# Kernel optimization log

Hardware: AMD Instinct MI355X
Metric: run time of the kernel (lower is better)

## Reference

```python
import jax, jax.numpy as jnp
import numpy as np


def _gather_neighbors(v, idx):
    # v: [B, N, D], idx: [B, N, K] -> [B, N, K, D]
    return jax.vmap(lambda vb, ib: vb[ib])(v, idx)


def setup_inputs() -> dict:
    key = jax.random.key(0)
    B, N, P, D, K = 8, 2048, 64, 128, 16
    ks = jax.random.split(key, 24)
    s = lambda fan_in: 1.0 / np.sqrt(fan_in)
    inp = {
        "x": jax.random.normal(ks[0], (B, N, 3), jnp.float32),
        "in_f": jax.random.normal(ks[1], (B, N, P), jnp.float32),
        "W_fc1": jax.random.normal(ks[2], (P, D), jnp.float32) * s(P),
        "b_fc1": jnp.zeros((D,), jnp.float32),
        "W_phi": jax.random.normal(ks[3], (D, D), jnp.float32) * s(D),
        "W_psi": jax.random.normal(ks[4], (D, D), jnp.float32) * s(D),
        "W_alpha": jax.random.normal(ks[5], (D, D), jnp.float32) * s(D),
        "W_dpt1": jax.random.normal(ks[6], (D, D), jnp.float32) * s(D),
        "b_dpt1": jnp.zeros((D,), jnp.float32),
        "W_dpt2": jax.random.normal(ks[7], (D, D), jnp.float32) * s(D),
        "b_dpt2": jnp.zeros((D,), jnp.float32),
        "W_gam1": jax.random.normal(ks[8], (D, D), jnp.float32) * s(D),
        "b_gam1": jnp.zeros((D,), jnp.float32),
        "W_gam2": jax.random.normal(ks[9], (D, D), jnp.float32) * s(D),
        "b_gam2": jnp.zeros((D,), jnp.float32),
        "W_del1": jax.random.normal(ks[10], (3, D), jnp.float32) * s(3),
        "b_del1": jnp.zeros((D,), jnp.float32),
        "W_del2": jax.random.normal(ks[11], (D, D), jnp.float32) * s(D),
        "b_del2": jnp.zeros((D,), jnp.float32),
        "W_fc2": jax.random.normal(ks[12], (D, P), jnp.float32) * s(D),
        "b_fc2": jnp.zeros((P,), jnp.float32),
        "k": K,
    }
    return inp


def reference(x, in_f, W_fc1, b_fc1, W_phi, W_psi, W_alpha,
              W_dpt1, b_dpt1, W_dpt2, b_dpt2,
              W_gam1, b_gam1, W_gam2, b_gam2,
              W_del1, b_del1, W_del2, b_del2,
              W_fc2, b_fc2, k):
    # squared pairwise distance [B, N, N] without [B,N,N,3] intermediate
    x2 = jnp.sum(x * x, axis=-1)                      # [B, N]
    d2 = x2[:, :, None] + x2[:, None, :] - 2.0 * jnp.einsum('bnc,bmc->bnm', x, x)
    knn_idx = jnp.argsort(d2, axis=-1)[:, :, :k]       # [B, N, K]

    points_knn = _gather_neighbors(x, knn_idx)         # [B, N, K, 3]
    f = in_f @ W_fc1 + b_fc1                           # [B, N, D]

    # positional encoding delta: MLP(x_i - x_j)
    diff = x[:, :, None, :] - points_knn               # [B, N, K, 3]
    delta = jax.nn.relu(diff @ W_del1 + b_del1) @ W_del2 + b_del2  # [B,N,K,D]

    psi = _gather_neighbors(f @ W_psi, knn_idx)        # [B, N, K, D]
    phi = (f @ W_phi)[:, :, None, :]                   # [B, N, 1, D]
    alpha = _gather_neighbors(f @ W_alpha, knn_idx)    # [B, N, K, D]
    dropped = (jax.nn.relu(f @ W_dpt1 + b_dpt1) @ W_dpt2 + b_dpt2)[:, :, None, :]

    pre = phi - psi + delta + dropped                  # [B, N, K, D]
    gamma = jax.nn.relu(pre @ W_gam1 + b_gam1) @ W_gam2 + b_gam2
    rho = jax.nn.softmax(gamma / jnp.sqrt(jnp.float32(k)), axis=2)

    y = jnp.sum(rho * (alpha + delta), axis=2)         # [B, N, D]
    return y @ W_fc2 + b_fc2 + in_f
```

## Files before the change

kernel.cpp:

```cpp
#include <hip/hip_runtime.h>
#include <hip/hip_bf16.h>
#include <math.h>

#define Bq 8
#define Nq 2048
#define Pq 64
#define Dq 128
#define Kq 16
#define BNq (Bq * Nq)

typedef unsigned short u16;
typedef __bf16 bf16x8v __attribute__((ext_vector_type(8)));
typedef float f32x4v __attribute__((ext_vector_type(4)));

__device__ __forceinline__ u16 f2b(float f) {
    return __builtin_bit_cast(u16, (__bf16)f);
}

#define OFF_DEL2 0
#define OFF_GAM1 16384
#define OFF_GAM2 32768
#define OFF_FC1  49152
#define OFF_PHI  57344
#define OFF_PSI  73728
#define OFF_ALF  90112
#define OFF_DPT1 106496
#define OFF_DPT2 122880
#define WT_TOTAL 139264

__global__ __launch_bounds__(256) void prep_kernel(
    const float* __restrict__ Wdel2, const float* __restrict__ Wgam1,
    const float* __restrict__ Wgam2, const float* __restrict__ Wfc1,
    const float* __restrict__ Wphi, const float* __restrict__ Wpsi,
    const float* __restrict__ Walpha, const float* __restrict__ Wdpt1,
    const float* __restrict__ Wdpt2, u16* __restrict__ Wt) {
    int idx = blockIdx.x * 256 + threadIdx.x;
    const float* W;
    int n, k;
    if (idx < OFF_FC1) {
        int m = idx >> 14, r = idx & 16383;
        W = (m == 0) ? Wdel2 : (m == 1) ? Wgam1 : Wgam2;
        n = r >> 7; k = r & 127;
    } else if (idx < OFF_PHI) {
        int r = idx - OFF_FC1;
        W = Wfc1; n = r >> 6; k = r & 63;
    } else {
        int r = idx - OFF_PHI;
        int m = r >> 14; r &= 16383;
        W = (m == 0) ? Wphi : (m == 1) ? Wpsi : (m == 2) ? Walpha : (m == 3) ? Wdpt1 : Wdpt2;
        n = r >> 7; k = r & 127;
    }
    Wt[idx] = f2b(W[k * 128 + n]);
}

__global__ __launch_bounds__(512) void knn_kernel(const float* __restrict__ x,
                                                  int* __restrict__ knn) {
    __shared__ float4 sx[Nq];
    __shared__ float sLd[32][16][17];
    __shared__ u16   sLi[32][16][17];
    const int b = blockIdx.x >> 6;
    const int q0 = (blockIdx.x & 63) * 32;
    const float* xb = x + b * Nq * 3;
    for (int j = threadIdx.x; j < Nq; j += 512) {
        float x0 = xb[j * 3 + 0], x1 = xb[j * 3 + 1], x2 = xb[j * 3 + 2];
        float n2 = __fadd_rn(__fadd_rn(__fmul_rn(x0, x0), __fmul_rn(x1, x1)),
                             __fmul_rn(x2, x2));
        sx[j] = make_float4(x0, x1, x2, n2);
    }
    __syncthreads();
    const int q = threadIdx.x & 31;
    const int sub = threadIdx.x >> 5;
    const float4 qv = sx[q0 + q];
    float bd[Kq];
    int bj[Kq];
#pragma unroll
    for (int s = 0; s < Kq; ++s) { bd[s] = INFINITY; bj[s] = 0x7fff; }
    const int j0 = sub * 128;
    for (int i = 0; i < 128; ++i) {
        const int j = j0 + i;
        float4 p = sx[j];
        float dot = __fadd_rn(__fadd_rn(__fmul_rn(qv.x, p.x), __fmul_rn(qv.y, p.y)),
                              __fmul_rn(qv.z, p.z));
        float d = __fsub_rn(__fadd_rn(qv.w, p.w), __fmul_rn(2.0f, dot));
        if (d < bd[Kq - 1]) {
            bd[Kq - 1] = d; bj[Kq - 1] = j;
#pragma unroll
            for (int s = Kq - 1; s >= 1; --s) {
                if (bd[s] < bd[s - 1]) {
                    float td = bd[s]; bd[s] = bd[s - 1]; bd[s - 1] = td;
                    int tj = bj[s]; bj[s] = bj[s - 1]; bj[s - 1] = tj;
                }
            }
        }
    }
#pragma unroll
    for (int s = 0; s < Kq; ++s) { sLd[q][sub][s] = bd[s]; sLi[q][sub][s] = (u16)bj[s]; }
    __syncthreads();
    if (threadIdx.x < 256) {
        const int mq = threadIdx.x & 31;
        const int s2 = threadIdx.x >> 5;
        float md[Kq]; int mi[Kq];
        int pa = 0, pb = 0;
#pragma unroll
        for (int i = 0; i < Kq; ++i) {
            float da = sLd[mq][2 * s2][pa], db = sLd[mq][2 * s2 + 1][pb];
            int ia = sLi[mq][2 * s2][pa], ib = sLi[mq][2 * s2 + 1][pb];
            bool ta = (da < db) || (da == db && ia < ib);
            md[i] = ta ? da : db; mi[i] = ta ? ia : ib;
            if (ta) ++pa; else ++pb;
        }
#pragma unroll
        for (int i = 0; i < Kq; ++i) { sLd[mq][2 * s2][i] = md[i]; sLi[mq][2 * s2][i] = (u16)mi[i]; }
    }
    __syncthreads();
    if (threadIdx.x < 32) {
        const int mq = threadIdx.x;
        int pos[8]; float hd[8]; int hi[8];
#pragma unroll
        for (int s = 0; s < 8; ++s) {
            pos[s] = 1; hd[s] = sLd[mq][2 * s][0]; hi[s] = sLi[mq][2 * s][0];
        }
        int* o = knn + (b * Nq + q0 + mq) * Kq;
#pragma unroll
        for (int oi = 0; oi < Kq; ++oi) {
            float bdv = hd[0]; int biv = hi[0]; int bs = 0;
#pragma unroll
            for (int s = 1; s < 8; ++s) {
                bool take = (hd[s] < bdv) || (hd[s] == bdv && hi[s] < biv);
                if (take) { bdv = hd[s]; biv = hi[s]; bs = s; }
            }
            o[oi] = biv;
#pragma unroll
            for (int s = 0; s < 8; ++s) {
                if (s == bs) {
                    int pp = pos[s] < Kq ? pos[s] : (Kq - 1);
                    bool ok = pos[s] < Kq;
                    hd[s] = ok ? sLd[mq][2 * s][pp] : INFINITY;
                    hi[s] = ok ? sLi[mq][2 * s][pp] : 0x7fffffff;
                    pos[s]++;
                }
            }
        }
    }
}

template <int BYTES, int ROWBYTES>
__device__ __forceinline__ void stageW(const u16* __restrict__ src,
                                       u16* __restrict__ sW, int t) {
#pragma unroll
    for (int c = 0; c < BYTES / 4096; ++c) {
        int lin = c * 4096 + t * 16;
        int n = lin / ROWBYTES;
        int o = lin % ROWBYTES;
        bf16x8v v = *(const bf16x8v*)((const char*)src + lin);
        *(bf16x8v*)((char*)sW + n * ROWBYTES + (o ^ ((n & 7) << 4))) = v;
    }
}

__device__ __forceinline__ void mfma_k128(const u16* __restrict__ sA,
                                          const u16* __restrict__ sW,
                                          int colbase, int lane,
                                          f32x4v (&acc)[4][2]) {
    const int kg = lane >> 4;
    const int l15 = lane & 15;
#pragma unroll
    for (int ks = 0; ks < 4; ++ks) {
        bf16x8v a[4], bfr[2];
#pragma unroll
        for (int m = 0; m < 4; ++m) {
            int row = m * 16 + l15;
            int o = (ks * 64 + kg * 16) ^ ((row & 7) << 4);
            a[m] = *(const bf16x8v*)((const char*)sA + row * 256 + o);
        }
#pragma unroll
        for (int nt = 0; nt < 2; ++nt) {
            int n = colbase + nt * 16 + l15;
            int o = (ks * 64 + kg * 16) ^ ((n & 7) << 4);
            bfr[nt] = *(const bf16x8v*)((const char*)sW + n * 256 + o);
        }
#pragma unroll
        for (int m = 0; m < 4; ++m)
#pragma unroll
            for (int nt = 0; nt < 2; ++nt)
                acc[m][nt] = __builtin_amdgcn_mfma_f32_16x16x32_bf16(a[m], bfr[nt], acc[m][nt], 0, 0, 0);
    }
}

__device__ __forceinline__ void mfma_k64(const u16* __restrict__ sA,
                                         const u16* __restrict__ sW,
                                         int colbase, int lane,
                                         f32x4v (&acc)[4][2]) {
    const int kg = lane >> 4;
    const int l15 = lane & 15;
#pragma unroll
    for (int ks = 0; ks < 2; ++ks) {
        bf16x8v a[4], bfr[2];
#pragma unroll
        for (int m = 0; m < 4; ++m) {
            int row = m * 16 + l15;
            int o = (ks * 64 + kg * 16) ^ ((row & 7) << 4);
            a[m] = *(const bf16x8v*)((const char*)sA + row * 128 + o);
        }
#pragma unroll
        for (int nt = 0; nt < 2; ++nt) {
            int n = colbase + nt * 16 + l15;
            int o = (ks * 64 + kg * 16) ^ ((n & 7) << 4);
            bfr[nt] = *(const bf16x8v*)((const char*)sW + n * 128 + o);
        }
#pragma unroll
        for (int m = 0; m < 4; ++m)
#pragma unroll
            for (int nt = 0; nt < 2; ++nt)
                acc[m][nt] = __builtin_amdgcn_mfma_f32_16x16x32_bf16(a[m], bfr[nt], acc[m][nt], 0, 0, 0);
    }
}

__global__ __launch_bounds__(256, 2) void feat_kernel(
    const float* __restrict__ in_f, const u16* __restrict__ Wt,
    const float* __restrict__ bfc1, const float* __restrict__ bdpt1,
    const float* __restrict__ bdpt2,
    float* __restrict__ base, u16* __restrict__ psiB, u16* __restrict__ alphaB) {
    __shared__ __align__(16) u16 sIn[64 * 64];
    __shared__ __align__(16) u16 sF[64 * 128];
    __shared__ __align__(16) u16 sW[128 * 128];
    const int t = threadIdx.x;
    const int lane = t & 63;
    const int w = t >> 6;
    const int kg = lane >> 4;
    const int l15 = lane & 15;
    const int p0 = blockIdx.x * 64;

    {
        const int r = t >> 2;
        const int c0 = (t & 3) * 16;
        const float* src = &in_f[(size_t)(p0 + r) * 64 + c0];
        float4 v0 = *(const float4*)(src + 0);
        float4 v1 = *(const float4*)(src + 4);
        float4 v2 = *(const float4*)(src + 8);
        float4 v3 = *(const float4*)(src + 12);
        bf16x8v lo, hi;
        lo[0] = (__bf16)v0.x; lo[1] = (__bf16)v0.y; lo[2] = (__bf16)v0.z; lo[3] = (__bf16)v0.w;
        lo[4] = (__bf16)v1.x; lo[5] = (__bf16)v1.y; lo[6] = (__bf16)v1.z; lo[7] = (__bf16)v1.w;
        hi[0] = (__bf16)v2.x; hi[1] = (__bf16)v2.y; hi[2] = (__bf16)v2.z; hi[3] = (__bf16)v2.w;
        hi[4] = (__bf16)v3.x; hi[5] = (__bf16)v3.y; hi[6] = (__bf16)v3.z; hi[7] = (__bf16)v3.w;
        const int swz = (r & 7) << 4;
        *(bf16x8v*)((char*)sIn + r * 128 + ((c0 * 2) ^ swz)) = lo;
        *(bf16x8v*)((char*)sIn + r * 128 + (((c0 + 8) * 2) ^ swz)) = hi;
    }

    f32x4v acc[4][2], accPhi[4][2];

    {
        float bv0 = bfc1[w * 32 + l15];
        float bv1 = bfc1[w * 32 + 16 + l15];
#pragma unroll
        for (int m = 0; m < 4; ++m) { acc[m][0] = f32x4v{bv0, bv0, bv0, bv0}; acc[m][1] = f32x4v{bv1, bv1, bv1, bv1}; }
    }
    stageW<16384, 128>(Wt + OFF_FC1, sW, t);
    __syncthreads();
    mfma_k64(sIn, sW, w * 32, lane, acc);

#pragma unroll
    for (int m = 0; m < 4; ++m)
#pragma unroll
        for (int nt = 0; nt < 2; ++nt)
#pragma unroll
            for (int rr = 0; rr < 4; ++rr) {
                int row = m * 16 + kg * 4 + rr;
                int col = w * 32 + nt * 16 + l15;
                *(__bf16*)((char*)sF + row * 256 + ((col * 2) ^ ((row & 7) << 4))) = (__bf16)acc[m][nt][rr];
            }

#pragma unroll
    for (int m = 0; m < 4; ++m) { accPhi[m][0] = f32x4v{0, 0, 0, 0}; accPhi[m][1] = f32x4v{0, 0, 0, 0}; }
    __syncthreads();
    stageW<32768, 256>(Wt + OFF_PHI, sW, t);
    __syncthreads();
    mfma_k128(sF, sW, w * 32, lane, accPhi);

#pragma unroll
    for (int m = 0; m < 4; ++m) { acc[m][0] = f32x4v{0, 0, 0, 0}; acc[m][1] = f32x4v{0, 0, 0, 0}; }
    __syncthreads();
    stageW<32768, 256>(Wt + OFF_PSI, sW, t);
    __syncthreads();
    mfma_k128(sF, sW, w * 32, lane, acc);
#pragma unroll
    for (int m = 0; m < 4; ++m)
#pragma unroll
        for (int nt = 0; nt < 2; ++nt)
#pragma unroll
            for (int rr = 0; rr < 4; ++rr) {
                int row = m * 16 + kg * 4 + rr;
                int col = w * 32 + nt * 16 + l15;
                psiB[(size_t)(p0 + row) * 128 + col] = f2b(acc[m][nt][rr]);
            }

#pragma unroll
    for (int m = 0; m < 4; ++m) { acc[m][0] = f32x4v{0, 0, 0, 0}; acc[m][1] = f32x4v{0, 0, 0, 0}; }
    __syncthreads();
    stageW<32768, 256>(Wt + OFF_ALF, sW, t);
    __syncthreads();
    mfma_k128(sF, sW, w * 32, lane, acc);
#pragma unroll
    for (int m = 0; m < 4; ++m)
#pragma unroll
        for (int nt = 0; nt < 2; ++nt)
#pragma unroll
            for (int rr = 0; rr < 4; ++rr) {
                int row = m * 16 + kg * 4 + rr;
                int col = w * 32 + nt * 16 + l15;
                alphaB[(size_t)(p0 + row) * 128 + col] = f2b(acc[m][nt][rr]);
            }

    {
        float bv0 = bdpt1[w * 32 + l15];
        float bv1 = bdpt1[w * 32 + 16 + l15];
#pragma unroll
        for (int m = 0; m < 4; ++m) { acc[m][0] = f32x4v{bv0, bv0, bv0, bv0}; acc[m][1] = f32x4v{bv1, bv1, bv1, bv1}; }
    }
    __syncthreads();
    stageW<32768, 256>(Wt + OFF_DPT1, sW, t);
    __syncthreads();
    mfma_k128(sF, sW, w * 32, lane, acc);
    __syncthreads();
#pragma unroll
    for (int m = 0; m < 4; ++m)
#pragma unroll
        for (int nt = 0; nt < 2; ++nt)
#pragma unroll
            for (int rr = 0; rr < 4; ++rr) {
                int row = m * 16 + kg * 4 + rr;
                int col = w * 32 + nt * 16 + l15;
                *(__bf16*)((char*)sF + row * 256 + ((col * 2) ^ ((row & 7) << 4))) =
                    (__bf16)fmaxf(acc[m][nt][rr], 0.f);
            }

    {
        float bv0 = bdpt2[w * 32 + l15];
        float bv1 = bdpt2[w * 32 + 16 + l15];
#pragma unroll
        for (int m = 0; m < 4; ++m) { acc[m][0] = f32x4v{bv0, bv0, bv0, bv0}; acc[m][1] = f32x4v{bv1, bv1, bv1, bv1}; }
    }
    __syncthreads();
    stageW<32768, 256>(Wt + OFF_DPT2, sW, t);
    __syncthreads();
    mfma_k128(sF, sW, w * 32, lane, acc);
#pragma unroll
    for (int m = 0; m < 4; ++m)
#pragma unroll
        for (int nt = 0; nt < 2; ++nt)
#pragma unroll
            for (int rr = 0; rr < 4; ++rr) {
                int row = m * 16 + kg * 4 + rr;
                int col = w * 32 + nt * 16 + l15;
                base[(size_t)(p0 + row) * 128 + col] = acc[m][nt][rr] + accPhi[m][nt][rr];
            }
}

__device__ __forceinline__ void mfma_n1(const u16* __restrict__ sA,
                                        const u16* __restrict__ sW,
                                        int colW, int kg, int l15,
                                        f32x4v (&acc)[4]) {
#pragma unroll
    for (int ks = 0; ks < 4; ++ks) {
        bf16x8v a[4], bb;
#pragma unroll
        for (int m = 0; m < 4; ++m) {
            int row = m * 16 + l15;
            int o = (ks * 64 + kg * 16) ^ ((row & 7) << 4);
            a[m] = *(const bf16x8v*)((const char*)sA + row * 256 + o);
        }
        {
            int o = (ks * 64 + kg * 16) ^ ((colW & 7) << 4);
            bb = *(const bf16x8v*)((const char*)sW + colW * 256 + o);
        }
#pragma unroll
        for (int m = 0; m < 4; ++m)
            acc[m] = __builtin_amdgcn_mfma_f32_16x16x32_bf16(a[m], bb, acc[m], 0, 0, 0);
    }
}

__global__ __launch_bounds__(512, 1) void main_kernel(
    const float* __restrict__ x, const float* __restrict__ in_f,
    const float* __restrict__ Wdel1, const float* __restrict__ bdel1,
    const float* __restrict__ bdel2,
    const float* __restrict__ bgam1, const float* __restrict__ bgam2,
    const float* __restrict__ Wfc2, const float* __restrict__ bfc2,
    const float* __restrict__ base, const u16* __restrict__ psiB,
    const u16* __restrict__ alphaB, const int* __restrict__ knn,
    const u16* __restrict__ Wt, float* __restrict__ out) {
    __shared__ __align__(16) u16 sW3[3][128 * 128];
    __shared__ __align__(16) u16 sA[64 * 128];
    __shared__ __align__(16) u16 sBP[64 * 128];
    __shared__ float sDiff[64][3];
    __shared__ int sIdx[64];
    __shared__ float sY[4][128];

    const int t = threadIdx.x;
    const int lane = t & 63;
    const int w = t >> 6;
    const int kg = lane >> 4;
    const int l15 = lane & 15;
    const int colW = w * 16 + l15;

#pragma unroll
    for (int s = 0; s < 3; ++s) {
        const u16* src = Wt + s * 16384;
        u16* dst = sW3[s];
#pragma unroll
        for (int c = 0; c < 4; ++c) {
            int lin = c * 8192 + t * 16;
            int n = lin >> 8;
            int o = lin & 255;
            bf16x8v v = *(const bf16x8v*)((const char*)src + lin);
            *(bf16x8v*)((char*)dst + n * 256 + (o ^ ((n & 7) << 4))) = v;
        }
    }
    const int hr = t >> 3;
    const int hc0 = (t & 7) * 16;
    float wdx[16], wdy[16], wdz[16], wdb[16];
#pragma unroll
    for (int c = 0; c < 4; ++c) {
        *(float4*)&wdx[c * 4] = *(const float4*)&Wdel1[0 * 128 + hc0 + c * 4];
        *(float4*)&wdy[c * 4] = *(const float4*)&Wdel1[1 * 128 + hc0 + c * 4];
        *(float4*)&wdz[c * 4] = *(const float4*)&Wdel1[2 * 128 + hc0 + c * 4];
        *(float4*)&wdb[c * 4] = *(const float4*)&bdel1[hc0 + c * 4];
    }
    const float bD = bdel2[colW];
    const float bG1 = bgam1[colW];
    const float bG2 = bgam2[colW];
    float bO = 0.f;
    if (t < 256) bO = bfc2[t & 63];

    const int pbase = blockIdx.x * 64;
    const int b = pbase >> 11;

    for (int chunk = 0; chunk < 16; ++chunk) {
        const int p0 = pbase + chunk * 4;
        if (t < 64) {
            int p = p0 + (t >> 4);
            int j = knn[p * Kq + (t & 15)];
            sIdx[t] = b * Nq + j;
            const float* xq = x + (size_t)p * 3;
            const float* xn = x + (size_t)(b * Nq + j) * 3;
            sDiff[t][0] = xq[0] - xn[0];
            sDiff[t][1] = xq[1] - xn[1];
            sDiff[t][2] = xq[2] - xn[2];
        }
        __syncthreads();

        bf16x8v aSt[2];
        {
            const float dx = sDiff[hr][0], dy = sDiff[hr][1], dz = sDiff[hr][2];
            const int nrow = sIdx[hr];
            const int prow = p0 + (hr >> 4);
            const int swz = (hr & 7) << 4;
#pragma unroll
            for (int hh = 0; hh < 2; ++hh) {
                const int c0 = hc0 + hh * 8;
                bf16x8v ps = *(const bf16x8v*)&psiB[(size_t)nrow * 128 + c0];
                float4 b0 = *(const float4*)&base[(size_t)prow * 128 + c0];
                float4 b1 = *(const float4*)&base[(size_t)prow * 128 + c0 + 4];
                aSt[hh] = *(const bf16x8v*)&alphaB[(size_t)nrow * 128 + c0];
                bf16x8v hv, bp;
#pragma unroll
                for (int j = 0; j < 8; ++j) {
                    int c = hh * 8 + j;
                    float v = fmaf(dz, wdz[c], fmaf(dy, wdy[c], fmaf(dx, wdx[c], wdb[c])));
                    hv[j] = (__bf16)fmaxf(v, 0.f);
                }
                bp[0] = (__bf16)(b0.x - (float)ps[0]); bp[1] = (__bf16)(b0.y - (float)ps[1]);
                bp[2] = (__bf16)(b0.z - (float)ps[2]); bp[3] = (__bf16)(b0.w - (float)ps[3]);
                bp[4] = (__bf16)(b1.x - (float)ps[4]); bp[5] = (__bf16)(b1.y - (float)ps[5]);
                bp[6] = (__bf16)(b1.z - (float)ps[6]); bp[7] = (__bf16)(b1.w - (float)ps[7]);
                const int ob = ((c0 * 2) ^ swz);
                *(bf16x8v*)((char*)sA + hr * 256 + ob) = hv;
                *(bf16x8v*)((char*)sBP + hr * 256 + ob) = bp;
            }
        }
        __syncthreads();

        f32x4v accD[4];
#pragma unroll
        for (int m = 0; m < 4; ++m) accD[m] = f32x4v{bD, bD, bD, bD};
        mfma_n1(sA, sW3[0], colW, kg, l15, accD);
        __syncthreads();

#pragma unroll
        for (int m = 0; m < 4; ++m)
#pragma unroll
            for (int rr = 0; rr < 4; ++rr) {
                int row = m * 16 + kg * 4 + rr;
                int off = row * 256 + ((colW * 2) ^ ((row & 7) << 4));
                float bpv = (float)*(const __bf16*)((const char*)sBP + off);
                *(__bf16*)((char*)sA + off) = (__bf16)(accD[m][rr] + bpv);
            }
        __syncthreads();

        {
            const int swz = (hr & 7) << 4;
            *(bf16x8v*)((char*)sBP + hr * 256 + ((hc0 * 2) ^ swz)) = aSt[0];
            *(bf16x8v*)((char*)sBP + hr * 256 + (((hc0 + 8) * 2) ^ swz)) = aSt[1];
        }
        f32x4v accT[4];
#pragma unroll
        for (int m = 0; m < 4; ++m) accT[m] = f32x4v{bG1, bG1, bG1, bG1};
        mfma_n1(sA, sW3[1], colW, kg, l15, accT);
        __syncthreads();

#pragma unroll
        for (int m = 0; m < 4; ++m)
#pragma unroll
            for (int rr = 0; rr < 4; ++rr) {
                int row = m * 16 + kg * 4 + rr;
                int off = row * 256 + ((colW * 2) ^ ((row & 7) << 4));
                *(__bf16*)((char*)sA + off) = (__bf16)fmaxf(accT[m][rr], 0.f);
            }
        __syncthreads();

#pragma unroll
        for (int m = 0; m < 4; ++m) accT[m] = f32x4v{bG2, bG2, bG2, bG2};
        mfma_n1(sA, sW3[2], colW, kg, l15, accT);

#pragma unroll
        for (int m = 0; m < 4; ++m) {
            float g0 = accT[m][0], g1v = accT[m][1], g2 = accT[m][2], g3 = accT[m][3];
            float mx = fmaxf(fmaxf(g0, g1v), fmaxf(g2, g3));
            mx = fmaxf(mx, __shfl_xor(mx, 16, 64));
            mx = fmaxf(mx, __shfl_xor(mx, 32, 64));
            float m4 = mx * 0.25f;
            float e0 = expf(0.25f * g0 - m4), e1 = expf(0.25f * g1v - m4);
            float e2 = expf(0.25f * g2 - m4), e3 = expf(0.25f * g3 - m4);
            float s = e0 + e1 + e2 + e3;
            s += __shfl_xor(s, 16, 64);
            s += __shfl_xor(s, 32, 64);
            float y = 0.f;
#pragma unroll
            for (int rr = 0; rr < 4; ++rr) {
                int row = m * 16 + kg * 4 + rr;
                int off = row * 256 + ((colW * 2) ^ ((row & 7) << 4));
                float al = (float)*(const __bf16*)((const char*)sBP + off);
                float ev = (rr == 0) ? e0 : (rr == 1) ? e1 : (rr == 2) ? e2 : e3;
                y = fmaf(ev, al + accD[m][rr], y);
            }
            y += __shfl_xor(y, 16, 64);
            y += __shfl_xor(y, 32, 64);
            if (kg == 0) sY[m][colW] = y / s;
        }
        __syncthreads();

        if (t < 256) {
            const int p = t >> 6;
            const int q = t & 63;
            const int gp = p0 + p;
            float a = bO + in_f[(size_t)gp * 64 + q];
#pragma unroll 8
            for (int d = 0; d < 128; ++d)
                a = fmaf(sY[p][d], Wfc2[d * 64 + q], a);
            out[(size_t)gp * 64 + q] = a;
        }
    }
}

extern "C" void kernel_launch(void* const* d_in, const int* in_sizes, int n_in,
                              void* d_out, int out_size, void* d_ws, size_t ws_size,
                              hipStream_t stream) {
    const float* x     = (const float*)d_in[0];
    const float* in_f  = (const float*)d_in[1];
    const float* Wfc1  = (const float*)d_in[2];
    const float* bfc1  = (const float*)d_in[3];
    const float* Wphi  = (const float*)d_in[4];
    const float* Wpsi  = (const float*)d_in[5];
    const float* Walpha= (const float*)d_in[6];
    const float* Wdpt1 = (const float*)d_in[7];
    const float* bdpt1 = (const float*)d_in[8];
    const float* Wdpt2 = (const float*)d_in[9];
    const float* bdpt2 = (const float*)d_in[10];
    const float* Wgam1 = (const float*)d_in[11];
    const float* bgam1 = (const float*)d_in[12];
    const float* Wgam2 = (const float*)d_in[13];
    const float* bgam2 = (const float*)d_in[14];
    const float* Wdel1 = (const float*)d_in[15];
    const float* bdel1 = (const float*)d_in[16];
    const float* Wdel2 = (const float*)d_in[17];
    const float* bdel2 = (const float*)d_in[18];
    const float* Wfc2  = (const float*)d_in[19];
    const float* bfc2  = (const float*)d_in[20];
    float* out = (float*)d_out;

    float* base   = (float*)d_ws;
    u16*   psiB   = (u16*)(base + (size_t)BNq * Dq);
    u16*   alphaB = psiB + (size_t)BNq * Dq;
    int*   knn    = (int*)(alphaB + (size_t)BNq * Dq);
    u16*   Wt     = (u16*)(knn + (size_t)BNq * Kq);

    prep_kernel<<<WT_TOTAL / 256, 256, 0, stream>>>(Wdel2, Wgam1, Wgam2, Wfc1, Wphi,
                                                    Wpsi, Walpha, Wdpt1, Wdpt2, Wt);
    knn_kernel<<<512, 512, 0, stream>>>(x, knn);
    feat_kernel<<<BNq / 64, 256, 0, stream>>>(in_f, Wt, bfc1, bdpt1, bdpt2,
                                              base, psiB, alphaB);
    main_kernel<<<256, 512, 0, stream>>>(x, in_f, Wdel1, bdel1, bdel2,
                                         bgam1, bgam2, Wfc2, bfc2,
                                         base, psiB, alphaB, knn, Wt, out);
}
```

Measured before the change: 290.0 us.

## Shrink main kernel LDS, hold gamma weights in registers, raise occupancy

The main kernel stops staging the two gamma weight matrices in shared memory. Each wave now keeps its column slice of W_gam1 and W_gam2 in registers, and psi and alpha are gathered straight from global memory at the point of use instead of through a staging buffer. This cuts LDS use enough for several blocks per CU, and the grid grows to BN/16 blocks of 4 chunks each, trading per-block weight staging for more parallelism. The KNN kernel halves its threads so each scans 256 candidates, dropping the pairwise merge stage; this adds register pressure and scattered global gathers.

```diff
diff --git a/kernel.cpp b/kernel.cpp
--- a/kernel.cpp
+++ b/kernel.cpp
@@ -15,6 +15,9 @@
 
 __device__ __forceinline__ u16 f2b(float f) {
     return __builtin_bit_cast(u16, (__bf16)f);
+}
+__device__ __forceinline__ float b2f(u16 u) {
+    return (float)__builtin_bit_cast(__bf16, u);
 }
 
 #define OFF_DEL2 0
@@ -53,15 +56,15 @@
     Wt[idx] = f2b(W[k * 128 + n]);
 }
 
-__global__ __launch_bounds__(512) void knn_kernel(const float* __restrict__ x,
+__global__ __launch_bounds__(256) void knn_kernel(const float* __restrict__ x,
                                                   int* __restrict__ knn) {
     __shared__ float4 sx[Nq];
-    __shared__ float sLd[32][16][17];
-    __shared__ u16   sLi[32][16][17];
+    __shared__ float sLd[32][8][17];
+    __shared__ int   sLi[32][8][17];
     const int b = blockIdx.x >> 6;
     const int q0 = (blockIdx.x & 63) * 32;
     const float* xb = x + b * Nq * 3;
-    for (int j = threadIdx.x; j < Nq; j += 512) {
+    for (int j = threadIdx.x; j < Nq; j += 256) {
         float x0 = xb[j * 3 + 0], x1 = xb[j * 3 + 1], x2 = xb[j * 3 + 2];
         float n2 = __fadd_rn(__fadd_rn(__fmul_rn(x0, x0), __fmul_rn(x1, x1)),
                              __fmul_rn(x2, x2));
@@ -74,9 +77,9 @@
     float bd[Kq];
     int bj[Kq];
 #pragma unroll
-    for (int s = 0; s < Kq; ++s) { bd[s] = INFINITY; bj[s] = 0x7fff; }
-    const int j0 = sub * 128;
-    for (int i = 0; i < 128; ++i) {
+    for (int s = 0; s < Kq; ++s) { bd[s] = INFINITY; bj[s] = 0; }
+    const int j0 = sub * 256;
+    for (int i = 0; i < 256; ++i) {
         const int j = j0 + i;
         float4 p = sx[j];
         float dot = __fadd_rn(__fadd_rn(__fmul_rn(qv.x, p.x), __fmul_rn(qv.y, p.y)),
@@ -94,31 +97,14 @@
         }
     }
 #pragma unroll
-    for (int s = 0; s < Kq; ++s) { sLd[q][sub][s] = bd[s]; sLi[q][sub][s] = (u16)bj[s]; }
-    __syncthreads();
-    if (threadIdx.x < 256) {
-        const int mq = threadIdx.x & 31;
-        const int s2 = threadIdx.x >> 5;
-        float md[Kq]; int mi[Kq];
-        int pa = 0, pb = 0;
-#pragma unroll
-        for (int i = 0; i < Kq; ++i) {
-            float da = sLd[mq][2 * s2][pa], db = sLd[mq][2 * s2 + 1][pb];
-            int ia = sLi[mq][2 * s2][pa], ib = sLi[mq][2 * s2 + 1][pb];
-            bool ta = (da < db) || (da == db && ia < ib);
-            md[i] = ta ? da : db; mi[i] = ta ? ia : ib;
-            if (ta) ++pa; else ++pb;
-        }
-#pragma unroll
-        for (int i = 0; i < Kq; ++i) { sLd[mq][2 * s2][i] = md[i]; sLi[mq][2 * s2][i] = (u16)mi[i]; }
-    }
+    for (int s = 0; s < Kq; ++s) { sLd[q][sub][s] = bd[s]; sLi[q][sub][s] = bj[s]; }
     __syncthreads();
     if (threadIdx.x < 32) {
         const int mq = threadIdx.x;
         int pos[8]; float hd[8]; int hi[8];
 #pragma unroll
         for (int s = 0; s < 8; ++s) {
-            pos[s] = 1; hd[s] = sLd[mq][2 * s][0]; hi[s] = sLi[mq][2 * s][0];
+            pos[s] = 1; hd[s] = sLd[mq][s][0]; hi[s] = sLi[mq][s][0];
         }
         int* o = knn + (b * Nq + q0 + mq) * Kq;
 #pragma unroll
@@ -135,8 +121,8 @@
                 if (s == bs) {
                     int pp = pos[s] < Kq ? pos[s] : (Kq - 1);
                     bool ok = pos[s] < Kq;
-                    hd[s] = ok ? sLd[mq][2 * s][pp] : INFINITY;
-                    hi[s] = ok ? sLi[mq][2 * s][pp] : 0x7fffffff;
+                    hd[s] = ok ? sLd[mq][s][pp] : INFINITY;
+                    hi[s] = ok ? sLi[mq][s][pp] : 0x7fffffff;
                     pos[s]++;
                 }
             }
@@ -357,10 +343,10 @@
             }
 }
 
-__device__ __forceinline__ void mfma_n1(const u16* __restrict__ sA,
-                                        const u16* __restrict__ sW,
-                                        int colW, int kg, int l15,
-                                        f32x4v (&acc)[4]) {
+__device__ __forceinline__ void mfma_ldsB(const u16* __restrict__ sA,
+                                          const u16* __restrict__ sW,
+                                          int colW, int kg, int l15,
+                                          f32x4v (&acc)[4]) {
 #pragma unroll
     for (int ks = 0; ks < 4; ++ks) {
         bf16x8v a[4], bb;
@@ -380,7 +366,23 @@
     }
 }
 
-__global__ __launch_bounds__(512, 1) void main_kernel(
+__device__ __forceinline__ void mfma_regB(const u16* __restrict__ sA,
+                                          const bf16x8v (&wB)[4],
+                                          int kg, int l15,
+                                          f32x4v (&acc)[4]) {
+#pragma unroll
+    for (int ks = 0; ks < 4; ++ks) {
+#pragma unroll
+        for (int m = 0; m < 4; ++m) {
+            int row = m * 16 + l15;
+            int o = (ks * 64 + kg * 16) ^ ((row & 7) << 4);
+            bf16x8v a = *(const bf16x8v*)((const char*)sA + row * 256 + o);
+            acc[m] = __builtin_amdgcn_mfma_f32_16x16x32_bf16(a, wB[ks], acc[m], 0, 0, 0);
+        }
+    }
+}
+
+__global__ __launch_bounds__(512, 4) void main_kernel(
     const float* __restrict__ x, const float* __restrict__ in_f,
     const float* __restrict__ Wdel1, const float* __restrict__ bdel1,
     const float* __restrict__ bdel2,
@@ -389,10 +391,9 @@
     const float* __restrict__ base, const u16* __restrict__ psiB,
     const u16* __restrict__ alphaB, const int* __restrict__ knn,
     const u16* __restrict__ Wt, float* __restrict__ out) {
-    __shared__ __align__(16) u16 sW3[3][128 * 128];
+    __shared__ __align__(16) u16 sWd2[128 * 128];
     __shared__ __align__(16) u16 sA[64 * 128];
-    __shared__ __align__(16) u16 sBP[64 * 128];
-    __shared__ float sDiff[64][3];
+    __shared__ float sWd1[512];
     __shared__ int sIdx[64];
     __shared__ float sY[4][128];
 
@@ -404,27 +405,23 @@
     const int colW = w * 16 + l15;
 
 #pragma unroll
-    for (int s = 0; s < 3; ++s) {
-        const u16* src = Wt + s * 16384;
-        u16* dst = sW3[s];
-#pragma unroll
-        for (int c = 0; c < 4; ++c) {
-            int lin = c * 8192 + t * 16;
-            int n = lin >> 8;
-            int o = lin & 255;
-            bf16x8v v = *(const bf16x8v*)((const char*)src + lin);
-            *(bf16x8v*)((char*)dst + n * 256 + (o ^ ((n & 7) << 4))) = v;
-        }
-    }
-    const int hr = t >> 3;
-    const int hc0 = (t & 7) * 16;
-    float wdx[16], wdy[16], wdz[16], wdb[16];
-#pragma unroll
     for (int c = 0; c < 4; ++c) {
-        *(float4*)&wdx[c * 4] = *(const float4*)&Wdel1[0 * 128 + hc0 + c * 4];
-        *(float4*)&wdy[c * 4] = *(const float4*)&Wdel1[1 * 128 + hc0 + c * 4];
-        *(float4*)&wdz[c * 4] = *(const float4*)&Wdel1[2 * 128 + hc0 + c * 4];
-        *(float4*)&wdb[c * 4] = *(const float4*)&bdel1[hc0 + c * 4];
+        int lin = c * 8192 + t * 16;
+        int n = lin >> 8;
+        int o = lin & 255;
+        bf16x8v v = *(const bf16x8v*)((const char*)(Wt + OFF_DEL2) + lin);
+        *(bf16x8v*)((char*)sWd2 + n * 256 + (o ^ ((n & 7) << 4))) = v;
+    }
+    {
+        int idx = t;
+        if (idx < 512) sWd1[idx] = (idx < 384) ? Wdel1[idx] : bdel1[idx - 384];
+    }
+    bf16x8v wG1[4], wG2[4];
+#pragma unroll
+    for (int ks = 0; ks < 4; ++ks) {
+        size_t off = (size_t)colW * 128 + ks * 32 + kg * 8;
+        wG1[ks] = *(const bf16x8v*)(Wt + OFF_GAM1 + off);
+        wG2[ks] = *(const bf16x8v*)(Wt + OFF_GAM2 + off);
     }
     const float bD = bdel2[colW];
     const float bG1 = bgam1[colW];
@@ -432,80 +429,71 @@
     float bO = 0.f;
     if (t < 256) bO = bfc2[t & 63];
 
-    const int pbase = blockIdx.x * 64;
+    const int pbase = blockIdx.x * 16;
     const int b = pbase >> 11;
-
-    for (int chunk = 0; chunk < 16; ++chunk) {
+    const int hr = t >> 3;
+    const int hc0 = (t & 7) * 16;
+
+    for (int chunk = 0; chunk < 4; ++chunk) {
         const int p0 = pbase + chunk * 4;
+
         if (t < 64) {
             int p = p0 + (t >> 4);
-            int j = knn[p * Kq + (t & 15)];
-            sIdx[t] = b * Nq + j;
+            sIdx[t] = b * Nq + knn[p * Kq + (t & 15)];
+        }
+
+        {
+            const int p = p0 + (hr >> 4);
+            const int j = knn[p * Kq + (hr & 15)];
             const float* xq = x + (size_t)p * 3;
             const float* xn = x + (size_t)(b * Nq + j) * 3;
-            sDiff[t][0] = xq[0] - xn[0];
-            sDiff[t][1] = xq[1] - xn[1];
-            sDiff[t][2] = xq[2] - xn[2];
+            const float dx = xq[0] - xn[0];
+            const float dy = xq[1] - xn[1];
+            const float dz = xq[2] - xn[2];
+            const int swzB = (hr & 7) << 4;
+#pragma unroll
+            for (int hh = 0; hh < 2; ++hh) {
+                bf16x8v hv;
+#pragma unroll
+                for (int c4 = 0; c4 < 2; ++c4) {
+                    const int cc = hc0 + hh * 8 + c4 * 4;
+                    float4 wx = *(const float4*)&sWd1[cc];
+                    float4 wy = *(const float4*)&sWd1[128 + cc];
+                    float4 wz = *(const float4*)&sWd1[256 + cc];
+                    float4 b4 = *(const float4*)&sWd1[384 + cc];
+                    hv[c4 * 4 + 0] = (__bf16)fmaxf(fmaf(dz, wz.x, fmaf(dy, wy.x, fmaf(dx, wx.x, b4.x))), 0.f);
+                    hv[c4 * 4 + 1] = (__bf16)fmaxf(fmaf(dz, wz.y, fmaf(dy, wy.y, fmaf(dx, wx.y, b4.y))), 0.f);
+                    hv[c4 * 4 + 2] = (__bf16)fmaxf(fmaf(dz, wz.z, fmaf(dy, wy.z, fmaf(dx, wx.z, b4.z))), 0.f);
+                    hv[c4 * 4 + 3] = (__bf16)fmaxf(fmaf(dz, wz.w, fmaf(dy, wy.w, fmaf(dx, wx.w, b4.w))), 0.f);
+                }
+                *(bf16x8v*)((char*)sA + hr * 256 + (((hc0 + hh * 8) * 2) ^ swzB)) = hv;
+            }
         }
         __syncthreads();
 
-        bf16x8v aSt[2];
-        {
-            const float dx = sDiff[hr][0], dy = sDiff[hr][1], dz = sDiff[hr][2];
-            const int nrow = sIdx[hr];
-            const int prow = p0 + (hr >> 4);
-            const int swz = (hr & 7) << 4;
-#pragma unroll
-            for (int hh = 0; hh < 2; ++hh) {
-                const int c0 = hc0 + hh * 8;
-                bf16x8v ps = *(const bf16x8v*)&psiB[(size_t)nrow * 128 + c0];
-                float4 b0 = *(const float4*)&base[(size_t)prow * 128 + c0];
-                float4 b1 = *(const float4*)&base[(size_t)prow * 128 + c0 + 4];
-                aSt[hh] = *(const bf16x8v*)&alphaB[(size_t)nrow * 128 + c0];
-                bf16x8v hv, bp;
-#pragma unroll
-                for (int j = 0; j < 8; ++j) {
-                    int c = hh * 8 + j;
-                    float v = fmaf(dz, wdz[c], fmaf(dy, wdy[c], fmaf(dx, wdx[c], wdb[c])));
-                    hv[j] = (__bf16)fmaxf(v, 0.f);
-                }
-                bp[0] = (__bf16)(b0.x - (float)ps[0]); bp[1] = (__bf16)(b0.y - (float)ps[1]);
-                bp[2] = (__bf16)(b0.z - (float)ps[2]); bp[3] = (__bf16)(b0.w - (float)ps[3]);
-                bp[4] = (__bf16)(b1.x - (float)ps[4]); bp[5] = (__bf16)(b1.y - (float)ps[5]);
-                bp[6] = (__bf16)(b1.z - (float)ps[6]); bp[7] = (__bf16)(b1.w - (float)ps[7]);
-                const int ob = ((c0 * 2) ^ swz);
-                *(bf16x8v*)((char*)sA + hr * 256 + ob) = hv;
-                *(bf16x8v*)((char*)sBP + hr * 256 + ob) = bp;
-            }
-        }
+        f32x4v accD[4];
+#pragma unroll
+        for (int m = 0; m < 4; ++m) accD[m] = f32x4v{bD, bD, bD, bD};
+        mfma_ldsB(sA, sWd2, colW, kg, l15, accD);
         __syncthreads();
 
-        f32x4v accD[4];
-#pragma unroll
-        for (int m = 0; m < 4; ++m) accD[m] = f32x4v{bD, bD, bD, bD};
-        mfma_n1(sA, sW3[0], colW, kg, l15, accD);
+#pragma unroll
+        for (int m = 0; m < 4; ++m) {
+            const float bs = base[(size_t)(p0 + m) * 128 + colW];
+#pragma unroll
+            for (int rr = 0; rr < 4; ++rr) {
+                int row = m * 16 + kg * 4 + rr;
+                float ps = b2f(psiB[(size_t)sIdx[row] * 128 + colW]);
+                int off = row * 256 + ((colW * 2) ^ ((row & 7) << 4));
+                *(__bf16*)((char*)sA + off) = (__bf16)(accD[m][rr] + (bs - ps));
+            }
+        }
         __syncthreads();
 
-#pragma unroll
-        for (int m = 0; m < 4; ++m)
-#pragma unroll
-            for (int rr = 0; rr < 4; ++rr) {
-                int row = m * 16 + kg * 4 + rr;
-                int off = row * 256 + ((colW * 2) ^ ((row & 7) << 4));
-                float bpv = (float)*(const __bf16*)((const char*)sBP + off);
-                *(__bf16*)((char*)sA + off) = (__bf16)(accD[m][rr] + bpv);
-            }
-        __syncthreads();
-
-        {
-            const int swz = (hr & 7) << 4;
-            *(bf16x8v*)((char*)sBP + hr * 256 + ((hc0 * 2) ^ swz)) = aSt[0];
-            *(bf16x8v*)((char*)sBP + hr * 256 + (((hc0 + 8) * 2) ^ swz)) = aSt[1];
-        }
         f32x4v accT[4];
 #pragma unroll
         for (int m = 0; m < 4; ++m) accT[m] = f32x4v{bG1, bG1, bG1, bG1};
-        mfma_n1(sA, sW3[1], colW, kg, l15, accT);
+        mfma_regB(sA, wG1, kg, l15, accT);
         __syncthreads();
 
 #pragma unroll
@@ -520,7 +508,7 @@
 
 #pragma unroll
         for (int m = 0; m < 4; ++m) accT[m] = f32x4v{bG2, bG2, bG2, bG2};
-        mfma_n1(sA, sW3[2], colW, kg, l15, accT);
+        mfma_regB(sA, wG2, kg, l15, accT);
 
 #pragma unroll
         for (int m = 0; m < 4; ++m) {
@@ -538,8 +526,7 @@
 #pragma unroll
             for (int rr = 0; rr < 4; ++rr) {
                 int row = m * 16 + kg * 4 + rr;
-                int off = row * 256 + ((colW * 2) ^ ((row & 7) << 4));
-                float al = (float)*(const __bf16*)((const char*)sBP + off);
+                float al = b2f(alphaB[(size_t)sIdx[row] * 128 + colW]);
                 float ev = (rr == 0) ? e0 : (rr == 1) ? e1 : (rr == 2) ? e2 : e3;
                 y = fmaf(ev, al + accD[m][rr], y);
             }
@@ -596,10 +583,10 @@
 
     prep_kernel<<<WT_TOTAL / 256, 256, 0, stream>>>(Wdel2, Wgam1, Wgam2, Wfc1, Wphi,
                                                     Wpsi, Walpha, Wdpt1, Wdpt2, Wt);
-    knn_kernel<<<512, 512, 0, stream>>>(x, knn);
+    knn_kernel<<<512, 256, 0, stream>>>(x, knn);
     feat_kernel<<<BNq / 64, 256, 0, stream>>>(in_f, Wt, bfc1, bdpt1, bdpt2,
                                               base, psiB, alphaB);
-    main_kernel<<<256, 512, 0, stream>>>(x, in_f, Wdel1, bdel1, bdel2,
-                                         bgam1, bgam2, Wfc2, bfc2,
-                                         base, psiB, alphaB, knn, Wt, out);
-}
+    main_kernel<<<BNq / 16, 512, 0, stream>>>(x, in_f, Wdel1, bdel1, bdel2,
+                                              bgam1, bgam2, Wfc2, bfc2,
+                                              base, psiB, alphaB, knn, Wt, out);
+}
```

Measured after the change: 254.2 us. 12.4% less time.
